# Kernel tuning notes

Measured on AMD Instinct MI355X. Metric: run time of the kernel, lower is better.

## Reference

```python
import jax, jax.numpy as jnp
import numpy as np

NUM_HEADS = 16
EPS = 1e-6  # LinearAttention.epsilon

def setup_inputs() -> dict:
    key = jax.random.key(0)
    ks = jax.random.split(key, 10)
    B, L, D = 4, 4096, 2048
    s = 1.0 / np.sqrt(D)
    x = jax.random.normal(ks[0], (B, L, D), dtype=jnp.float32)
    attention_mask = jnp.ones((B, L), dtype=jnp.float32)
    Wq = jax.random.normal(ks[1], (D, D), dtype=jnp.float32) * s
    bq = jnp.zeros((D,), dtype=jnp.float32)
    Wk = jax.random.normal(ks[2], (D, D), dtype=jnp.float32) * s
    bk = jnp.zeros((D,), dtype=jnp.float32)
    Wv = jax.random.normal(ks[3], (D, D), dtype=jnp.float32) * s
    bv = jnp.zeros((D,), dtype=jnp.float32)
    Wo = jax.random.normal(ks[4], (D, D), dtype=jnp.float32) * s
    bo = jnp.zeros((D,), dtype=jnp.float32)
    return {"x": x, "attention_mask": attention_mask, "Wq": Wq, "bq": bq,
            "Wk": Wk, "bk": bk, "Wv": Wv, "bv": bv, "Wo": Wo, "bo": bo}

def reference(x, attention_mask, Wq, bq, Wk, bk, Wv, bv, Wo, bo):
    B, L, Dm = x.shape
    H = NUM_HEADS
    Dh = Dm // H
    # q/k/v projections -> [B, H, L, Dh]
    def proj(W, b):
        return (x @ W + b).reshape(B, L, H, Dh).transpose(0, 2, 1, 3)
    q = proj(Wq, bq)
    k = proj(Wk, bk)
    v = proj(Wv, bv)
    # feature map: elu(x) + 1
    q = jax.nn.elu(q) + 1.0
    k = jax.nn.elu(k) + 1.0
    # mask keys/values: mask [B, 1, L, 1]
    m = attention_mask[:, None, :, None]
    k = k * m
    v = v * m
    # causal linear attention via cumulative sums over sequence dim
    k_cum = jnp.cumsum(k, axis=2)          # [B,H,L,Dh]
    kv_cum = jnp.cumsum(k * v, axis=2)     # [B,H,L,Dh] (diagonal kv state, as in source)
    z = jnp.sum(q * k_cum, axis=-1) + EPS  # [B,H,L]
    z = z * attention_mask[:, None, :]
    out = (q * kv_cum) / z[..., None]      # [B,H,L,Dh]
    out = out.transpose(0, 2, 1, 3).reshape(B, L, Dm)
    return out @ Wo + bo
```

## Files before the change

### kernel.cpp

```cpp
#include <hip/hip_runtime.h>
#include <cstdint>
#include <cstddef>

#define EPS_F 1e-6f

__device__ inline unsigned short f2bf(float f) {
    union { float f; unsigned u; } v; v.f = f;
    unsigned r = v.u + 0x7fffu + ((v.u >> 16) & 1u);
    return (unsigned short)(r >> 16);
}
__device__ inline float bf2f(unsigned u16) {
    union { unsigned u; float f; } v; v.u = u16 << 16; return v.f;
}

typedef __attribute__((ext_vector_type(8))) __bf16 bf16x8;
typedef __attribute__((ext_vector_type(8))) short short8;
typedef __attribute__((ext_vector_type(8))) unsigned short ushort8;
typedef __attribute__((ext_vector_type(4))) float floatx4;
typedef __attribute__((ext_vector_type(4))) unsigned uintx4;

__device__ inline void async_load16(const void* g, void* l) {
    __builtin_amdgcn_global_load_lds((const __attribute__((address_space(1))) void*)g,
                                     (__attribute__((address_space(3))) void*)l,
                                     16, 0, 0);
}

#define LDS_OFF(p) ((unsigned)(unsigned long long)(const __attribute__((address_space(3))) void*)(p))

__global__ void cast_x_kernel(const float* __restrict__ in, unsigned short* __restrict__ out, int n8) {
    int i = blockIdx.x * blockDim.x + threadIdx.x;
    if (i < n8) {
        float4 a = ((const float4*)in)[2 * i];
        float4 b = ((const float4*)in)[2 * i + 1];
        short8 o;
        o[0] = (short)f2bf(a.x); o[1] = (short)f2bf(a.y);
        o[2] = (short)f2bf(a.z); o[3] = (short)f2bf(a.w);
        o[4] = (short)f2bf(b.x); o[5] = (short)f2bf(b.y);
        o[6] = (short)f2bf(b.z); o[7] = (short)f2bf(b.w);
        ((short8*)out)[i] = o;
    }
}

__global__ void transpose_cast_kernel(const float* __restrict__ W0, const float* __restrict__ W1,
                                      const float* __restrict__ W2, const float* __restrict__ W3,
                                      unsigned short* __restrict__ WtBase, int n) {
    const float* W = (blockIdx.z == 0) ? W0 : (blockIdx.z == 1) ? W1 : (blockIdx.z == 2) ? W2 : W3;
    unsigned short* Wt = WtBase + (size_t)blockIdx.z * n * n;
    __shared__ float tile[32][33];
    int bx = blockIdx.x * 32;
    int by = blockIdx.y * 32;
    int tx = threadIdx.x;
    int ty = threadIdx.y;
    #pragma unroll
    for (int i = 0; i < 32; i += 8)
        tile[ty + i][tx] = W[(size_t)(by + ty + i) * n + bx + tx];
    __syncthreads();
    #pragma unroll
    for (int i = 0; i < 32; i += 8)
        Wt[(size_t)(bx + ty + i) * n + by + tx] = f2bf(tile[tx][ty + i]);
}

#define BMT 256
#define BNT 256
#define BKT 32
#define SLOT_ELEMS (BMT * BKT)
#define SLOT_BYTES 16384
#define DMODEL 2048

#define DSR(dst, base, OFF) \
    asm volatile("ds_read_b128 %0, %1 offset:" OFF : "=v"(dst) : "v"(base) : "memory")
#define READ_A0(f, base) { DSR(f[0], base, "0");    DSR(f[1], base, "1024"); \
                           DSR(f[2], base, "2048"); DSR(f[3], base, "3072"); }
#define READ_A1(f, base) { DSR(f[0], base, "4096"); DSR(f[1], base, "5120"); \
                           DSR(f[2], base, "6144"); DSR(f[3], base, "7168"); }
#define READ_B(f, base)  { DSR(f[0], base, "0");    DSR(f[1], base, "1024"); \
                           DSR(f[2], base, "2048"); DSR(f[3], base, "3072"); }

#define MFMA_HALF(i0, af, bf)                                                   \
    _Pragma("unroll")                                                           \
    for (int i_ = 0; i_ < 4; i_++) {                                            \
        bf16x8 a_ = __builtin_bit_cast(bf16x8, af[i_]);                         \
        _Pragma("unroll")                                                       \
        for (int j_ = 0; j_ < 4; j_++)                                          \
            acc[i0 + i_][j_] = __builtin_amdgcn_mfma_f32_16x16x32_bf16(         \
                a_, __builtin_bit_cast(bf16x8, bf[j_]), acc[i0 + i_][j_], 0, 0, 0); \
    }

#define GEMM_ITER(T, BCUR, BNXT)                                                \
  {                                                                             \
    const int T_ = (T);                                                         \
    if (T_ <= NT - 3)      asm volatile("s_waitcnt vmcnt(4)" ::: "memory");     \
    else if (T_ == NT - 2) asm volatile("s_waitcnt vmcnt(0)" ::: "memory");     \
    __builtin_amdgcn_s_barrier();                                               \
    __builtin_amdgcn_sched_barrier(0);                                          \
    if (T_ + 3 < NT) stage(T_ + 3, (T_ + 3) & 3);                               \
    asm volatile("s_waitcnt lgkmcnt(4)" ::: "memory");                          \
    __builtin_amdgcn_sched_barrier(0);                                          \
    __builtin_amdgcn_s_setprio(1);                                              \
    MFMA_HALF(0, af0, BCUR);                                                    \
    __builtin_amdgcn_s_setprio(0);                                              \
    const int tn_ = T_ + 1;                                                     \
    const unsigned aN_ = aLane + (unsigned)((tn_ & 3) * SLOT_BYTES);            \
    const unsigned bN_ = bLane + (unsigned)((tn_ & 3) * SLOT_BYTES);            \
    if (tn_ < NT) {                                                             \
      READ_A0(af0, aN_);                                                        \
      READ_B(BNXT, bN_);                                                        \
      asm volatile("s_waitcnt lgkmcnt(8)" ::: "memory");                        \
    } else {                                                                    \
      asm volatile("s_waitcnt lgkmcnt(0)" ::: "memory");                        \
    }                                                                           \
    __builtin_amdgcn_sched_barrier(0);                                          \
    __builtin_amdgcn_s_setprio(1);                                              \
    MFMA_HALF(4, af1, BCUR);                                                    \
    __builtin_amdgcn_s_setprio(0);                                              \
    if (tn_ < NT) { READ_A1(af1, aN_); }                                        \
  }

template<int FINAL>
__global__ __launch_bounds__(512, 2)
void gemm_kernel(const unsigned short* __restrict__ A,
                 const unsigned short* __restrict__ Bt,
                 const float* __restrict__ b0, const float* __restrict__ b1,
                 const float* __restrict__ b2,
                 const float* __restrict__ mask,
                 unsigned short* __restrict__ qo, unsigned short* __restrict__ ko,
                 unsigned short* __restrict__ vo,
                 float* __restrict__ Cf,
                 int M, int K) {
    __shared__ __align__(16) unsigned short As[4 * SLOT_ELEMS];
    __shared__ __align__(16) unsigned short Bs[4 * SLOT_ELEMS];

    const int tid  = threadIdx.x;
    const int lane = tid & 63;
    const int wave = tid >> 6;
    const int wr   = wave >> 2;
    const int wc   = wave & 3;
    const int quad  = lane >> 4;
    const int row16 = lane & 15;

    const int nwg = (int)(gridDim.x * gridDim.y);
    const int bid = (int)(blockIdx.y * gridDim.x + blockIdx.x);
    const int cpx = nwg >> 3;
    const int swz = (bid & 7) * cpx + (bid >> 3);
    const int bm  = swz % (int)gridDim.x;
    const int bn  = swz / (int)gridDim.x;

    const int m0    = bm * BMT;
    const int nglob = bn * BNT;
    int mat = 0, n0 = nglob;
    const float* bias = b0;
    unsigned short* Cb = nullptr;
    if (!FINAL) {
        mat  = nglob >> 11;
        n0   = nglob & (DMODEL - 1);
        bias = (mat == 0) ? b0 : (mat == 1) ? b1 : b2;
        Cb   = (mat == 0) ? qo : (mat == 1) ? ko : vo;
    }

    floatx4 acc[8][4] = {};

    const unsigned short* gA[2];
    const unsigned short* gB[2];
    #pragma unroll
    for (int b = 0; b < 2; b++) {
        int s = b * 512 + tid;
        int r = s >> 2, c = s & 3;
        int cg = c ^ ((r >> 1) & 3);
        gA[b] = A  + (size_t)(m0 + r) * K + cg * 8;
        gB[b] = Bt + (size_t)(nglob + r) * K + cg * 8;
    }

    const unsigned asB = LDS_OFF(As);
    const unsigned bsB = LDS_OFF(Bs);
    const unsigned cP    = (unsigned)(quad ^ ((row16 >> 1) & 3));
    const unsigned aLane = asB + (unsigned)(wr * 8192 + row16 * 64) + cP * 16u;
    const unsigned bLane = bsB + (unsigned)(wc * 4096 + row16 * 64) + cP * 16u;

    auto stage = [&](int tt, int sl) {
        const int koff = tt * BKT;
        #pragma unroll
        for (int b = 0; b < 2; b++) {
            int s = b * 512 + tid;
            async_load16(gA[b] + koff, As + sl * SLOT_ELEMS + s * 8);
            async_load16(gB[b] + koff, Bs + sl * SLOT_ELEMS + s * 8);
        }
    };

    const int NT = K / BKT;
    stage(0, 0); stage(1, 1); stage(2, 2);
    asm volatile("s_waitcnt vmcnt(8)" ::: "memory");
    __builtin_amdgcn_s_barrier();
    __builtin_amdgcn_sched_barrier(0);

    uintx4 af0[4], af1[4], bfE[4], bfO[4];
    READ_A0(af0, aLane);
    READ_B(bfE, bLane);
    READ_A1(af1, aLane);

    for (int t = 0; t < NT; t += 2) {
        GEMM_ITER(t,     bfE, bfO);
        GEMM_ITER(t + 1, bfO, bfE);
    }

    float bcache[4];
    #pragma unroll
    for (int j = 0; j < 4; j++) bcache[j] = bias[n0 + wc * 64 + j * 16 + row16];
    #pragma unroll
    for (int i = 0; i < 8; i++) {
        #pragma unroll
        for (int r = 0; r < 4; r++) {
            int row = m0 + wr * 128 + i * 16 + quad * 4 + r;
            float mr = 1.0f;
            if (!FINAL && mat >= 1) mr = mask[row];
            #pragma unroll
            for (int j = 0; j < 4; j++) {
                int col = n0 + wc * 64 + j * 16 + row16;
                float v = acc[i][j][r] + bcache[j];
                if (FINAL) {
                    Cf[(size_t)row * DMODEL + col] = v;
                } else {
                    if (mat <= 1) v = (v > 0.f) ? (v + 1.f) : __expf(v);
                    v *= mr;
                    Cb[(size_t)row * DMODEL + col] = f2bf(v);
                }
            }
        }
    }
}

#define SL    4096
#define SD    2048
#define SH    16
#define CHUNK 64
#define NCH   64

__global__ void scan_partial_kernel(const unsigned short* __restrict__ k,
                                    const unsigned short* __restrict__ v,
                                    float* __restrict__ sumK, float* __restrict__ sumKV) {
    int blk = blockIdx.x;
    int c = blk & (NCH - 1), bh = blk >> 6;
    int b = bh >> 4, h = bh & (SH - 1);
    int lane = threadIdx.x;
    int tg = lane >> 4, dg = lane & 15;
    size_t base = ((size_t)(b * SL + c * CHUNK + tg)) * SD + h * 128 + dg * 8;
    float sk[8] = {0.f, 0.f, 0.f, 0.f, 0.f, 0.f, 0.f, 0.f};
    float skv[8] = {0.f, 0.f, 0.f, 0.f, 0.f, 0.f, 0.f, 0.f};
    for (int it = 0; it < CHUNK / 4; it++) {
        ushort8 kw = *(const ushort8*)(k + base);
        ushort8 vw = *(const ushort8*)(v + base);
        #pragma unroll
        for (int j = 0; j < 8; j++) {
            float kf = bf2f(kw[j]);
            float vf = bf2f(vw[j]);
            sk[j] += kf; skv[j] += kf * vf;
        }
        base += (size_t)4 * SD;
    }
    #pragma unroll
    for (int j = 0; j < 8; j++) {
        sk[j]  += __shfl_xor(sk[j], 16);  sk[j]  += __shfl_xor(sk[j], 32);
        skv[j] += __shfl_xor(skv[j], 16); skv[j] += __shfl_xor(skv[j], 32);
    }
    if (tg == 0) {
        size_t o = ((size_t)bh * NCH + c) * 128 + dg * 8;
        *(float4*)(sumK  + o)     = make_float4(sk[0], sk[1], sk[2], sk[3]);
        *(float4*)(sumK  + o + 4) = make_float4(sk[4], sk[5], sk[6], sk[7]);
        *(float4*)(sumKV + o)     = make_float4(skv[0], skv[1], skv[2], skv[3]);
        *(float4*)(sumKV + o + 4) = make_float4(skv[4], skv[5], skv[6], skv[7]);
    }
}

__global__ void scan_offsets_kernel(const float* __restrict__ sumK, const float* __restrict__ sumKV,
                                    float* __restrict__ offK, float* __restrict__ offKV) {
    int bh = blockIdx.x;
    int d  = threadIdx.x;
    float aK = 0.f, aKV = 0.f;
    for (int c = 0; c < NCH; c++) {
        size_t o = ((size_t)bh * NCH + c) * 128 + d;
        float sk = sumK[o], skv = sumKV[o];
        offK[o] = aK; offKV[o] = aKV;
        aK += sk; aKV += skv;
    }
}

__global__ void scan_final_kernel(const unsigned short* __restrict__ q,
                                  const unsigned short* __restrict__ k,
                                  const unsigned short* __restrict__ v,
                                  const float* __restrict__ offK, const float* __restrict__ offKV,
                                  const float* __restrict__ mask,
                                  unsigned short* __restrict__ out) {
    int blk = blockIdx.x;
    int c = blk & (NCH - 1), bh = blk >> 6;
    int b = bh >> 4, h = bh & (SH - 1);
    int lane = threadIdx.x;
    size_t ob = ((size_t)bh * NCH + c) * 128 + 2 * lane;
    float2 kcv = *(const float2*)(offK  + ob);
    float2 kvv = *(const float2*)(offKV + ob);
    float kc0 = kcv.x, kc1 = kcv.y, kv0 = kvv.x, kv1 = kvv.y;
    size_t base = ((size_t)(b * SL + c * CHUNK)) * SD + h * 128 + 2 * lane;
    const float* mrow = mask + (size_t)b * SL + c * CHUNK;
    for (int s = 0; s < CHUNK / 4; s++) {
        unsigned kw[4], vw[4], qw[4];
        #pragma unroll
        for (int u = 0; u < 4; u++) {
            size_t a = base + (size_t)u * SD;
            kw[u] = *(const unsigned*)(k + a);
            vw[u] = *(const unsigned*)(v + a);
            qw[u] = *(const unsigned*)(q + a);
        }
        float p[4], n0[4], n1[4];
        #pragma unroll
        for (int u = 0; u < 4; u++) {
            float kk0 = bf2f(kw[u] & 0xffff), kk1 = bf2f(kw[u] >> 16);
            float vv0 = bf2f(vw[u] & 0xffff), vv1 = bf2f(vw[u] >> 16);
            float qq0 = bf2f(qw[u] & 0xffff), qq1 = bf2f(qw[u] >> 16);
            kc0 += kk0; kc1 += kk1;
            kv0 += kk0 * vv0; kv1 += kk1 * vv1;
            p[u]  = qq0 * kc0 + qq1 * kc1;
            n0[u] = qq0 * kv0; n1[u] = qq1 * kv1;
        }
        #pragma unroll
        for (int off = 32; off > 0; off >>= 1) {
            #pragma unroll
            for (int u = 0; u < 4; u++) p[u] += __shfl_xor(p[u], off);
        }
        #pragma unroll
        for (int u = 0; u < 4; u++) {
            float z = (p[u] + EPS_F) * mrow[s * 4 + u];
            float inv = 1.0f / z;
            unsigned o0 = f2bf(n0[u] * inv);
            unsigned o1 = f2bf(n1[u] * inv);
            *(unsigned*)(out + base + (size_t)u * SD) = o0 | (o1 << 16);
        }
        base += (size_t)4 * SD;
    }
}

extern "C" void kernel_launch(void* const* d_in, const int* in_sizes, int n_in,
                              void* d_out, int out_size, void* d_ws, size_t ws_size,
                              hipStream_t stream) {
    const float* x  = (const float*)d_in[0];
    const float* am = (const float*)d_in[1];
    const float* Wq = (const float*)d_in[2];
    const float* bq = (const float*)d_in[3];
    const float* Wk = (const float*)d_in[4];
    const float* bk = (const float*)d_in[5];
    const float* Wv = (const float*)d_in[6];
    const float* bv = (const float*)d_in[7];
    const float* Wo = (const float*)d_in[8];
    const float* bo = (const float*)d_in[9];
    float* out = (float*)d_out;

    const int Bb = 4, L = 4096, D = 2048;
    const int M = Bb * L;
    const size_t MD = (size_t)M * D;

    char* w = (char*)d_ws;
    unsigned short* xb    = (unsigned short*)w; w += MD * 2;
    unsigned short* qb    = (unsigned short*)w; w += MD * 2;
    unsigned short* kb    = (unsigned short*)w; w += MD * 2;
    unsigned short* vb    = (unsigned short*)w; w += MD * 2;
    unsigned short* WT    = (unsigned short*)w; w += (size_t)4 * D * D * 2;
    float* sumK  = (float*)w; w += (size_t)64 * NCH * 128 * 4;
    float* sumKV = (float*)w; w += (size_t)64 * NCH * 128 * 4;
    float* offK  = (float*)w; w += (size_t)64 * NCH * 128 * 4;
    float* offKV = (float*)w; w += (size_t)64 * NCH * 128 * 4;
    unsigned short* attnb = xb;

    int n8 = (int)(MD / 8);
    cast_x_kernel<<<(n8 + 255) / 256, 256, 0, stream>>>(x, xb, n8);
    dim3 tb(32, 8);
    dim3 tg(D / 32, D / 32, 4);
    transpose_cast_kernel<<<tg, tb, 0, stream>>>(Wq, Wk, Wv, Wo, WT, D);

    dim3 gq(M / BMT, 3 * D / BNT);
    gemm_kernel<0><<<gq, 512, 0, stream>>>(xb, WT, bq, bk, bv, am, qb, kb, vb, nullptr, M, D);

    scan_partial_kernel<<<64 * NCH, 64, 0, stream>>>(kb, vb, sumK, sumKV);
    scan_offsets_kernel<<<64, 128, 0, stream>>>(sumK, sumKV, offK, offKV);
    scan_final_kernel<<<64 * NCH, 64, 0, stream>>>(qb, kb, vb, offK, offKV, am, attnb);

    dim3 go(M / BMT, D / BNT);
    gemm_kernel<1><<<go, 512, 0, stream>>>(attnb, WT + (size_t)3 * D * D, bo, nullptr, nullptr,
                                           nullptr, nullptr, nullptr, nullptr, out, M, D);
}
```

Before: 889.2 us.

## Replace QKV GEMM with simple 128x128 kernel and retune scan kernels

Swaps the heavily pipelined 256x256 four-stage QKV GEMM for a simpler 128x128x64 kernel with a single LDS buffer and syncthreads per K step, aiming for more workgroups across the device. The output GEMM keeps the tuned 256x256 path under a new name. The scan offsets kernel is split over two blocks per head and preloads 32 chunk sums at a time. The final scan kernel now handles two heads per block with 4-wide loads. The unpipelined QKV GEMM exposes global-load latency, since loads are not overlapped with MFMA work.

```diff
diff --git a/kernel.cpp b/kernel.cpp
--- a/kernel.cpp
+++ b/kernel.cpp
@@ -60,12 +60,101 @@
         Wt[(size_t)(bx + ty + i) * n + by + tx] = f2bf(tile[tx][ty + i]);
 }
 
-#define BMT 256
-#define BNT 256
-#define BKT 32
-#define SLOT_ELEMS (BMT * BKT)
-#define SLOT_BYTES 16384
+#define BMT 128
+#define BNT 128
+#define BKT 64
 #define DMODEL 2048
+
+__global__ __launch_bounds__(256, 2)
+void gemm_qkv(const unsigned short* __restrict__ A,
+              const unsigned short* __restrict__ Bt,
+              const float* __restrict__ b0, const float* __restrict__ b1,
+              const float* __restrict__ b2,
+              const float* __restrict__ mask,
+              unsigned short* __restrict__ qo, unsigned short* __restrict__ ko,
+              unsigned short* __restrict__ vo,
+              int M, int K) {
+    __shared__ __align__(16) unsigned short As[BMT * BKT];
+    __shared__ __align__(16) unsigned short Bs[BNT * BKT];
+
+    const int tid  = threadIdx.x;
+    const int wave = tid >> 6;
+    const int lane = tid & 63;
+    const int m0    = blockIdx.x * BMT;
+    const int nglob = blockIdx.y * BNT;
+    const int mat  = nglob >> 11;
+    const int n0   = nglob & (DMODEL - 1);
+    const float* bias = (mat == 0) ? b0 : (mat == 1) ? b1 : b2;
+    unsigned short* Cb = (mat == 0) ? qo : (mat == 1) ? ko : vo;
+
+    const int wm = (wave >> 1) * 64;
+    const int wn = (wave & 1) * 64;
+    const int quad  = lane >> 4;
+    const int row16 = lane & 15;
+
+    floatx4 acc[4][4] = {};
+
+    const int srow_lo = lane >> 3;
+    const int schunk  = lane & 7;
+
+    for (int k0 = 0; k0 < K; k0 += BKT) {
+        #pragma unroll
+        for (int i = 0; i < 4; i++) {
+            int slot_base = wave * 256 + i * 64;
+            int r  = wave * 32 + i * 8 + srow_lo;
+            int cg = schunk ^ (r & 7);
+            const unsigned short* ga = A  + (size_t)(m0 + r) * K + k0 + cg * 8;
+            const unsigned short* gb = Bt + (size_t)(nglob + r) * K + k0 + cg * 8;
+            async_load16(ga, As + (size_t)slot_base * 8);
+            async_load16(gb, Bs + (size_t)slot_base * 8);
+        }
+        __syncthreads();
+
+        #pragma unroll
+        for (int kk = 0; kk < 2; kk++) {
+            bf16x8 af[4], bfr[4];
+            #pragma unroll
+            for (int t = 0; t < 4; t++) {
+                int ra = wm + t * 16 + row16;
+                int ca = (kk * 4 + quad) ^ (ra & 7);
+                af[t]  = __builtin_bit_cast(bf16x8, *(const short8*)(As + (size_t)ra * 64 + ca * 8));
+                int rb = wn + t * 16 + row16;
+                int cb = (kk * 4 + quad) ^ (rb & 7);
+                bfr[t] = __builtin_bit_cast(bf16x8, *(const short8*)(Bs + (size_t)rb * 64 + cb * 8));
+            }
+            #pragma unroll
+            for (int i = 0; i < 4; i++)
+                #pragma unroll
+                for (int j = 0; j < 4; j++)
+                    acc[i][j] = __builtin_amdgcn_mfma_f32_16x16x32_bf16(af[i], bfr[j], acc[i][j], 0, 0, 0);
+        }
+        __syncthreads();
+    }
+
+    float bcache[4];
+    #pragma unroll
+    for (int j = 0; j < 4; j++) bcache[j] = bias[n0 + wn + j * 16 + row16];
+    #pragma unroll
+    for (int i = 0; i < 4; i++) {
+        #pragma unroll
+        for (int r = 0; r < 4; r++) {
+            int row = m0 + wm + i * 16 + quad * 4 + r;
+            float mr = (mat >= 1) ? mask[row] : 1.0f;
+            #pragma unroll
+            for (int j = 0; j < 4; j++) {
+                int col = n0 + wn + j * 16 + row16;
+                float v = acc[i][j][r] + bcache[j];
+                if (mat <= 1) v = (v > 0.f) ? (v + 1.f) : __expf(v);
+                v *= mr;
+                Cb[(size_t)row * DMODEL + col] = f2bf(v);
+            }
+        }
+    }
+}
+
+#define FBK 32
+#define FSLOT_ELEMS (256 * FBK)
+#define FSLOT_BYTES 16384
 
 #define DSR(dst, base, OFF) \
     asm volatile("ds_read_b128 %0, %1 offset:" OFF : "=v"(dst) : "v"(base) : "memory")
@@ -100,8 +189,8 @@
     MFMA_HALF(0, af0, BCUR);                                                    \
     __builtin_amdgcn_s_setprio(0);                                              \
     const int tn_ = T_ + 1;                                                     \
-    const unsigned aN_ = aLane + (unsigned)((tn_ & 3) * SLOT_BYTES);            \
-    const unsigned bN_ = bLane + (unsigned)((tn_ & 3) * SLOT_BYTES);            \
+    const unsigned aN_ = aLane + (unsigned)((tn_ & 3) * FSLOT_BYTES);           \
+    const unsigned bN_ = bLane + (unsigned)((tn_ & 3) * FSLOT_BYTES);           \
     if (tn_ < NT) {                                                             \
       READ_A0(af0, aN_);                                                        \
       READ_B(BNXT, bN_);                                                        \
@@ -116,19 +205,14 @@
     if (tn_ < NT) { READ_A1(af1, aN_); }                                        \
   }
 
-template<int FINAL>
 __global__ __launch_bounds__(512, 2)
-void gemm_kernel(const unsigned short* __restrict__ A,
-                 const unsigned short* __restrict__ Bt,
-                 const float* __restrict__ b0, const float* __restrict__ b1,
-                 const float* __restrict__ b2,
-                 const float* __restrict__ mask,
-                 unsigned short* __restrict__ qo, unsigned short* __restrict__ ko,
-                 unsigned short* __restrict__ vo,
-                 float* __restrict__ Cf,
-                 int M, int K) {
-    __shared__ __align__(16) unsigned short As[4 * SLOT_ELEMS];
-    __shared__ __align__(16) unsigned short Bs[4 * SLOT_ELEMS];
+void gemm_final(const unsigned short* __restrict__ A,
+                const unsigned short* __restrict__ Bt,
+                const float* __restrict__ bias,
+                float* __restrict__ Cf,
+                int M, int K) {
+    __shared__ __align__(16) unsigned short As[4 * FSLOT_ELEMS];
+    __shared__ __align__(16) unsigned short Bs[4 * FSLOT_ELEMS];
 
     const int tid  = threadIdx.x;
     const int lane = tid & 63;
@@ -145,17 +229,8 @@
     const int bm  = swz % (int)gridDim.x;
     const int bn  = swz / (int)gridDim.x;
 
-    const int m0    = bm * BMT;
-    const int nglob = bn * BNT;
-    int mat = 0, n0 = nglob;
-    const float* bias = b0;
-    unsigned short* Cb = nullptr;
-    if (!FINAL) {
-        mat  = nglob >> 11;
-        n0   = nglob & (DMODEL - 1);
-        bias = (mat == 0) ? b0 : (mat == 1) ? b1 : b2;
-        Cb   = (mat == 0) ? qo : (mat == 1) ? ko : vo;
-    }
+    const int m0 = bm * 256;
+    const int n0 = bn * 256;
 
     floatx4 acc[8][4] = {};
 
@@ -167,7 +242,7 @@
         int r = s >> 2, c = s & 3;
         int cg = c ^ ((r >> 1) & 3);
         gA[b] = A  + (size_t)(m0 + r) * K + cg * 8;
-        gB[b] = Bt + (size_t)(nglob + r) * K + cg * 8;
+        gB[b] = Bt + (size_t)(n0 + r) * K + cg * 8;
     }
 
     const unsigned asB = LDS_OFF(As);
@@ -177,16 +252,16 @@
     const unsigned bLane = bsB + (unsigned)(wc * 4096 + row16 * 64) + cP * 16u;
 
     auto stage = [&](int tt, int sl) {
-        const int koff = tt * BKT;
+        const int koff = tt * FBK;
         #pragma unroll
         for (int b = 0; b < 2; b++) {
             int s = b * 512 + tid;
-            async_load16(gA[b] + koff, As + sl * SLOT_ELEMS + s * 8);
-            async_load16(gB[b] + koff, Bs + sl * SLOT_ELEMS + s * 8);
+            async_load16(gA[b] + koff, As + sl * FSLOT_ELEMS + s * 8);
+            async_load16(gB[b] + koff, Bs + sl * FSLOT_ELEMS + s * 8);
         }
     };
 
-    const int NT = K / BKT;
+    const int NT = K / FBK;
     stage(0, 0); stage(1, 1); stage(2, 2);
     asm volatile("s_waitcnt vmcnt(8)" ::: "memory");
     __builtin_amdgcn_s_barrier();
@@ -210,19 +285,10 @@
         #pragma unroll
         for (int r = 0; r < 4; r++) {
             int row = m0 + wr * 128 + i * 16 + quad * 4 + r;
-            float mr = 1.0f;
-            if (!FINAL && mat >= 1) mr = mask[row];
             #pragma unroll
             for (int j = 0; j < 4; j++) {
                 int col = n0 + wc * 64 + j * 16 + row16;
-                float v = acc[i][j][r] + bcache[j];
-                if (FINAL) {
-                    Cf[(size_t)row * DMODEL + col] = v;
-                } else {
-                    if (mat <= 1) v = (v > 0.f) ? (v + 1.f) : __expf(v);
-                    v *= mr;
-                    Cb[(size_t)row * DMODEL + col] = f2bf(v);
-                }
+                Cf[(size_t)row * DMODEL + col] = acc[i][j][r] + bcache[j];
             }
         }
     }
@@ -270,16 +336,27 @@
     }
 }
 
-__global__ void scan_offsets_kernel(const float* __restrict__ sumK, const float* __restrict__ sumKV,
-                                    float* __restrict__ offK, float* __restrict__ offKV) {
-    int bh = blockIdx.x;
-    int d  = threadIdx.x;
+__global__ __launch_bounds__(64)
+void scan_offsets_kernel(const float* __restrict__ sumK, const float* __restrict__ sumKV,
+                         float* __restrict__ offK, float* __restrict__ offKV) {
+    int blk = blockIdx.x;
+    int bh  = blk >> 1;
+    int d   = (blk & 1) * 64 + threadIdx.x;
     float aK = 0.f, aKV = 0.f;
-    for (int c = 0; c < NCH; c++) {
-        size_t o = ((size_t)bh * NCH + c) * 128 + d;
-        float sk = sumK[o], skv = sumKV[o];
-        offK[o] = aK; offKV[o] = aKV;
-        aK += sk; aKV += skv;
+    #pragma unroll 1
+    for (int h = 0; h < 2; h++) {
+        float vK[32], vKV[32];
+        #pragma unroll
+        for (int c2 = 0; c2 < 32; c2++) {
+            size_t o = ((size_t)bh * NCH + h * 32 + c2) * 128 + d;
+            vK[c2] = sumK[o]; vKV[c2] = sumKV[o];
+        }
+        #pragma unroll
+        for (int c2 = 0; c2 < 32; c2++) {
+            size_t o = ((size_t)bh * NCH + h * 32 + c2) * 128 + d;
+            offK[o]  = aK;  aK  += vK[c2];
+            offKV[o] = aKV; aKV += vKV[c2];
+        }
     }
 }
 
@@ -290,37 +367,54 @@
                                   const float* __restrict__ mask,
                                   unsigned short* __restrict__ out) {
     int blk = blockIdx.x;
-    int c = blk & (NCH - 1), bh = blk >> 6;
-    int b = bh >> 4, h = bh & (SH - 1);
+    int c   = blk & (NCH - 1);
+    int bhp = blk >> 6;
+    int b = bhp >> 3, hp = bhp & 7;
     int lane = threadIdx.x;
-    size_t ob = ((size_t)bh * NCH + c) * 128 + 2 * lane;
-    float2 kcv = *(const float2*)(offK  + ob);
-    float2 kvv = *(const float2*)(offKV + ob);
-    float kc0 = kcv.x, kc1 = kcv.y, kv0 = kvv.x, kv1 = kvv.y;
-    size_t base = ((size_t)(b * SL + c * CHUNK)) * SD + h * 128 + 2 * lane;
+    int half = lane >> 5, dq = lane & 31;
+    int h  = hp * 2 + half;
+    int bh = b * SH + h;
+
+    size_t ob = ((size_t)bh * NCH + c) * 128 + dq * 4;
+    float4 kc4 = *(const float4*)(offK  + ob);
+    float4 kv4 = *(const float4*)(offKV + ob);
+    float kc[4] = {kc4.x, kc4.y, kc4.z, kc4.w};
+    float kv[4] = {kv4.x, kv4.y, kv4.z, kv4.w};
+
+    size_t base = ((size_t)(b * SL + c * CHUNK)) * SD + h * 128 + dq * 4;
     const float* mrow = mask + (size_t)b * SL + c * CHUNK;
+
     for (int s = 0; s < CHUNK / 4; s++) {
-        unsigned kw[4], vw[4], qw[4];
+        uint2 kw[4], vw[4], qw[4];
         #pragma unroll
         for (int u = 0; u < 4; u++) {
             size_t a = base + (size_t)u * SD;
-            kw[u] = *(const unsigned*)(k + a);
-            vw[u] = *(const unsigned*)(v + a);
-            qw[u] = *(const unsigned*)(q + a);
-        }
-        float p[4], n0[4], n1[4];
+            kw[u] = *(const uint2*)(k + a);
+            vw[u] = *(const uint2*)(v + a);
+            qw[u] = *(const uint2*)(q + a);
+        }
+        float p[4], nn[4][4];
         #pragma unroll
         for (int u = 0; u < 4; u++) {
-            float kk0 = bf2f(kw[u] & 0xffff), kk1 = bf2f(kw[u] >> 16);
-            float vv0 = bf2f(vw[u] & 0xffff), vv1 = bf2f(vw[u] >> 16);
-            float qq0 = bf2f(qw[u] & 0xffff), qq1 = bf2f(qw[u] >> 16);
-            kc0 += kk0; kc1 += kk1;
-            kv0 += kk0 * vv0; kv1 += kk1 * vv1;
-            p[u]  = qq0 * kc0 + qq1 * kc1;
-            n0[u] = qq0 * kv0; n1[u] = qq1 * kv1;
-        }
-        #pragma unroll
-        for (int off = 32; off > 0; off >>= 1) {
+            float kf[4], vf[4], qf[4];
+            kf[0] = bf2f(kw[u].x & 0xffff); kf[1] = bf2f(kw[u].x >> 16);
+            kf[2] = bf2f(kw[u].y & 0xffff); kf[3] = bf2f(kw[u].y >> 16);
+            vf[0] = bf2f(vw[u].x & 0xffff); vf[1] = bf2f(vw[u].x >> 16);
+            vf[2] = bf2f(vw[u].y & 0xffff); vf[3] = bf2f(vw[u].y >> 16);
+            qf[0] = bf2f(qw[u].x & 0xffff); qf[1] = bf2f(qw[u].x >> 16);
+            qf[2] = bf2f(qw[u].y & 0xffff); qf[3] = bf2f(qw[u].y >> 16);
+            float pu = 0.f;
+            #pragma unroll
+            for (int j = 0; j < 4; j++) {
+                kc[j] += kf[j];
+                kv[j] += kf[j] * vf[j];
+                pu += qf[j] * kc[j];
+                nn[u][j] = qf[j] * kv[j];
+            }
+            p[u] = pu;
+        }
+        #pragma unroll
+        for (int off = 16; off > 0; off >>= 1) {
             #pragma unroll
             for (int u = 0; u < 4; u++) p[u] += __shfl_xor(p[u], off);
         }
@@ -328,9 +422,12 @@
         for (int u = 0; u < 4; u++) {
             float z = (p[u] + EPS_F) * mrow[s * 4 + u];
             float inv = 1.0f / z;
-            unsigned o0 = f2bf(n0[u] * inv);
-            unsigned o1 = f2bf(n1[u] * inv);
-            *(unsigned*)(out + base + (size_t)u * SD) = o0 | (o1 << 16);
+            uint2 o2;
+            unsigned lo0 = f2bf(nn[u][0] * inv), hi0 = f2bf(nn[u][1] * inv);
+            unsigned lo1 = f2bf(nn[u][2] * inv), hi1 = f2bf(nn[u][3] * inv);
+            o2.x = lo0 | (hi0 << 16);
+            o2.y = lo1 | (hi1 << 16);
+            *(uint2*)(out + base + (size_t)u * SD) = o2;
         }
         base += (size_t)4 * SD;
     }
@@ -374,13 +471,12 @@
     transpose_cast_kernel<<<tg, tb, 0, stream>>>(Wq, Wk, Wv, Wo, WT, D);
 
     dim3 gq(M / BMT, 3 * D / BNT);
-    gemm_kernel<0><<<gq, 512, 0, stream>>>(xb, WT, bq, bk, bv, am, qb, kb, vb, nullptr, M, D);
+    gemm_qkv<<<gq, 256, 0, stream>>>(xb, WT, bq, bk, bv, am, qb, kb, vb, M, D);
 
     scan_partial_kernel<<<64 * NCH, 64, 0, stream>>>(kb, vb, sumK, sumKV);
-    scan_offsets_kernel<<<64, 128, 0, stream>>>(sumK, sumKV, offK, offKV);
-    scan_final_kernel<<<64 * NCH, 64, 0, stream>>>(qb, kb, vb, offK, offKV, am, attnb);
-
-    dim3 go(M / BMT, D / BNT);
-    gemm_kernel<1><<<go, 512, 0, stream>>>(attnb, WT + (size_t)3 * D * D, bo, nullptr, nullptr,
-                                           nullptr, nullptr, nullptr, nullptr, out, M, D);
-}
+    scan_offsets_kernel<<<128, 64, 0, stream>>>(sumK, sumKV, offK, offKV);
+    scan_final_kernel<<<2048, 64, 0, stream>>>(qb, kb, vb, offK, offKV, am, attnb);
+
+    dim3 go(M / 256, D / 256);
+    gemm_final<<<go, 512, 0, stream>>>(attnb, WT + (size_t)3 * D * D, bo, out, M, D);
+}
```

New measurement: 896.2 us. Within noise of the previous version (+0.8%).
